# Kernel optimization log

Measured on AMD Instinct MI355X. Metric: run time of the kernel, lower is better.

Reference implementation:

```python
import jax, jax.numpy as jnp
import numpy as np

N_NODES = 1_000_000
N_EDGES = 16_000_000
ALPHA = 0.85
MAX_ITER = 100
TOL = 1e-6


def setup_inputs() -> dict:
    key = jax.random.key(0)
    k1, k2 = jax.random.split(key)
    x = jax.random.normal(k1, (N_NODES,), dtype=jnp.float32)
    edge_index = jax.random.randint(k2, (2, N_EDGES), 0, N_NODES, dtype=jnp.int64)
    return {"x": x, "edge_index": edge_index}


def reference(x, edge_index):
    N = x.shape[0]
    rows = edge_index[0]  # destination (row index of sparse M)
    cols = edge_index[1]  # source (column index; out-degree normalization)

    # values of M*alpha: alpha / out_degree(col), gathered per edge
    deg = jax.ops.segment_sum(jnp.ones_like(cols, dtype=jnp.float32), cols,
                              num_segments=N)  # torch.bincount(columns)
    vals = ALPHA / deg[cols]  # [E]; div-by-zero -> inf, matching torch

    inv_n = jnp.float32(1.0) / N
    teleport = (1.0 - ALPHA) * inv_n
    v0 = jnp.full((N,), inv_n, dtype=jnp.float32)
    thresh = jnp.float32(N) * TOL

    def step(carry, _):
        v, done = carry
        # SpMV: out[row] += vals * v[col]
        new_v = jax.ops.segment_sum(vals * v[cols], rows, num_segments=N) + teleport
        err = jnp.abs(new_v - v).sum()
        v_next = jnp.where(done, v, new_v)
        done_next = done | (err < thresh)
        return (v_next, done_next), None

    (v, _), _ = jax.lax.scan(step, (v0, jnp.array(False)), None, length=MAX_ITER)
    return v
```

## Files before the change

kernel.cpp:

```cpp
#include <hip/hip_runtime.h>
#include <hip/hip_cooperative_groups.h>

namespace cg = cooperative_groups;


static constexpr int   NN       = 1000000;
static constexpr int   NE       = 16000000;
static constexpr float ALPHA    = 0.85f;
static constexpr int   MAX_ITER = 100;
static constexpr float THRESH   = 1.0f;
static constexpr float INV_N    = 1.0f / 1000000.0f;
static constexpr float TELEPORT = 0.15f * (1.0f / 1000000.0f);
static constexpr float SCALE    = 8796093022208.0f;
static constexpr float INVSCALE = 1.0f / 8796093022208.0f;

static constexpr int T     = 256;
static constexpr int T5    = 512;
static constexpr int NCH   = 2048;
static constexpr int BSH   = 14;
static constexpr int BKN   = 16384;
static constexpr int NBK   = 64;
static constexpr int NBKU  = 62;
static constexpr int NSUBB = 496;
static constexpr int NSLC  = 489;
static constexpr int NK4A  = 124;

static constexpr size_t OFF_WCG  = 0;
static constexpr size_t OFF_WR8  = 64002048;
static constexpr size_t OFF_PACC = 80002560;
static constexpr size_t OFF_CNTR = 112508416;
static constexpr size_t OFF_CNTC = 113032704;
static constexpr size_t OFF_CTRL = 113556992;
static constexpr size_t OFF_RDEG = 113561088;
static constexpr size_t OFF_W    = 117561088;
static constexpr size_t NEED     = 121561120;

typedef int      vi4 __attribute__((ext_vector_type(4)));
typedef unsigned vu4 __attribute__((ext_vector_type(4)));

template<typename TT>
__device__ __forceinline__ TT ntload(const TT* p) { return __builtin_nontemporal_load(p); }

struct P {
    unsigned* wcg; unsigned char* wr8; unsigned short* colp;
    int* pacc; unsigned* cntR; unsigned* cntC;
    float* rdeg; float* w;
    unsigned* totR; unsigned* totC; unsigned* baseR; unsigned* baseC;
    unsigned* flags; int* ovf; float* errF;
};
__device__ __forceinline__ P mk(char* ws) {
    P p;
    p.wcg  = (unsigned*)(ws + OFF_WCG);
    p.wr8  = (unsigned char*)(ws + OFF_WR8);
    p.colp = (unsigned short*)(ws + OFF_PACC);
    p.pacc = (int*)(ws + OFF_PACC);
    p.cntR = (unsigned*)(ws + OFF_CNTR);
    p.cntC = (unsigned*)(ws + OFF_CNTC);
    unsigned* ctrl = (unsigned*)(ws + OFF_CTRL);
    p.rdeg = (float*)(ws + OFF_RDEG);
    p.w    = (float*)(ws + OFF_W);
    p.totR = ctrl; p.totC = ctrl + 64; p.baseR = ctrl + 128; p.baseC = ctrl + 200;
    p.flags = ctrl + 280; p.ovf = (int*)(ctrl + 281); p.errF = (float*)(ctrl + 288);
    return p;
}

__device__ void atomic_fallback(cg::grid_group& grid, int is64,
                                const int* e32, const long long* e64,
                                int* ai, int* deg, float* rdeg,
                                float* vA, float* vB, float* w,
                                float* err, float* out,
                                int tid, int stride, int th)
{
    for (int i = tid; i < NN; i += stride) { ai[i] = 0; deg[i] = 0; vA[i] = INV_N; }
    grid.sync();
    if (is64) { const long long* cols = e64 + NE;
        for (int e = tid; e < NE; e += stride) atomicAdd(&deg[(int)cols[e]], 1); }
    else      { const int* cols = e32 + NE;
        for (int e = tid; e < NE; e += stride) atomicAdd(&deg[cols[e]], 1); }
    grid.sync();
    for (int i = tid; i < NN; i += stride) rdeg[i] = ALPHA / (float)deg[i];
    grid.sync();
    float* v = vA; float* nv = vB;
    for (int iter = 0; iter < MAX_ITER; ++iter) {
        for (int i = tid; i < NN; i += stride) { w[i] = v[i] * rdeg[i]; ai[i] = 0; }
        grid.sync();
        if (is64) { const long long* rows = e64; const long long* cols = e64 + NE;
            for (int e = tid; e < NE; e += stride)
                atomicAdd(&ai[(int)rows[e]], __float2int_rn(w[(int)cols[e]] * SCALE)); }
        else { const int* rows = e32; const int* cols = e32 + NE;
            for (int e = tid; e < NE; e += stride)
                atomicAdd(&ai[rows[e]], __float2int_rn(w[cols[e]] * SCALE)); }
        grid.sync();
        float pe = 0.0f;
        for (int i = tid; i < NN; i += stride) {
            float x = TELEPORT + (float)ai[i] * INVSCALE;
            pe += fabsf(x - v[i]); nv[i] = x;
        }
        #pragma unroll
        for (int off = 32; off > 0; off >>= 1) pe += __shfl_down(pe, off, 64);
        if ((th & 63) == 0) unsafeAtomicAdd(&err[iter], pe);
        grid.sync();
        float e = ((volatile float*)err)[iter];
        float* t = v; v = nv; nv = t;
        if (e < THRESH) break;
    }
    for (int i = tid; i < NN; i += stride) out[i] = v[i];
}

__global__ __launch_bounds__(256) void k0_init(const int* __restrict__ e32, char* ws)
{
    P p = mk(ws);
    __shared__ int snz;
    const int th = threadIdx.x;
    if (th == 0) snz = 0;
    __syncthreads();
    if (e32[2 * th + 1] != 0) atomicOr(&snz, 1);
    __syncthreads();
    if (th == 0) { p.flags[0] = (snz == 0) ? 1u : 0u; *p.ovf = 0; p.w[NN] = 0.0f; }
    if (th < MAX_ITER) p.errF[th] = 0.0f;
}

__global__ __launch_bounds__(256, 8) void k1_hist(const int* __restrict__ e32, char* ws)
{
    P p = mk(ws);
    if (p.flags[0]) return;
    __shared__ int h[128];
    const int th = threadIdx.x, blk = blockIdx.x;
    const int e0 = (int)(((long long)NE * blk) >> 11);
    const int e1 = (int)(((long long)NE * (blk + 1)) >> 11);
    if (th < 128) h[th] = 0;
    __syncthreads();
    const vi4* R4 = (const vi4*)e32;
    const vi4* C4 = (const vi4*)(e32 + NE);
    const int qe = (e1 + 3) >> 2;
    for (int q = (e0 >> 2) + th; q < qe; q += T) {
        vi4 R = R4[q], C = C4[q];
        int rr[4] = {R.x, R.y, R.z, R.w}, cc[4] = {C.x, C.y, C.z, C.w};
        #pragma unroll
        for (int j = 0; j < 4; ++j) {
            int e = 4 * q + j;
            if (e >= e0 && e < e1) {
                atomicAdd(&h[rr[j] >> BSH], 1);
                atomicAdd(&h[64 + (cc[j] >> BSH)], 1);
            }
        }
    }
    __syncthreads();
    if (th < 64) {
        p.cntR[(size_t)th * NCH + blk] = (unsigned)h[th];
        p.cntC[(size_t)th * NCH + blk] = (unsigned)h[64 + th];
    }
}

__global__ __launch_bounds__(256, 4) void k2_scan(char* ws)
{
    P p = mk(ws);
    if (p.flags[0]) return;
    __shared__ int S[256];
    const int th = threadIdx.x, blk = blockIdx.x;
    const int side = blk >> 6, b = blk & 63;
    unsigned* cnt = (side ? p.cntC : p.cntR) + (size_t)b * NCH;
    unsigned v[8]; unsigned s = 0;
    #pragma unroll
    for (int i = 0; i < 8; ++i) { v[i] = cnt[8 * th + i]; s += v[i]; }
    S[th] = (int)s; __syncthreads();
    for (int off = 1; off < 256; off <<= 1) {
        int x = (th >= off) ? S[th - off] : 0;
        __syncthreads(); S[th] += x; __syncthreads();
    }
    unsigned run = (unsigned)S[th] - s;
    #pragma unroll
    for (int i = 0; i < 8; ++i) { unsigned t = v[i]; cnt[8 * th + i] = run; run += t; }
    if (th == 255) (side ? p.totC : p.totR)[b] = run;
}

__global__ __launch_bounds__(256) void k2b_bases(char* ws)
{
    P p = mk(ws);
    if (p.flags[0]) return;
    __shared__ int S[128];
    const int th = threadIdx.x;
    unsigned pt = 0;
    if (th < 128) {
        unsigned t = (th < 64) ? p.totR[th] : p.totC[th - 64];
        pt = (t + 7u) & ~7u;
        S[th] = (int)pt;
    }
    __syncthreads();
    for (int off = 1; off < 64; off <<= 1) {
        int x = (th < 128 && (th & 63) >= off) ? S[th - off] : 0;
        __syncthreads(); if (th < 128) S[th] += x; __syncthreads();
    }
    if (th < 64) {
        p.baseR[th] = (unsigned)S[th] - pt;
        if (th == 63) p.baseR[64] = (unsigned)S[63];
    } else if (th < 128) {
        p.baseC[th - 64] = (unsigned)S[th] - pt;
        if (th == 127) p.baseC[64] = (unsigned)S[127];
    }
    __syncthreads();
    if (th < 64) {
        unsigned tot = p.totC[th], bs = p.baseC[th], pp = (tot + 7u) & ~7u;
        for (unsigned i = tot; i < pp; ++i) p.colp[bs + i] = 0;
    }
}

__global__ __launch_bounds__(256, 2) void k3ab_scat(const int* __restrict__ e32, char* ws)
{
    P p = mk(ws);
    if (p.flags[0]) return;
    __shared__ int SH3[14720];
    unsigned short* pcL  = (unsigned short*)SH3;
    int*            wcL  = SH3 + 4096;
    unsigned char*  wr8L = (unsigned char*)(SH3 + 12288);
    int* cFill = SH3 + 14336; int* cFlsh = SH3 + 14400; int* cWpos = SH3 + 14464;
    int* rFill = SH3 + 14528; int* rFlsh = SH3 + 14592; int* rWpos = SH3 + 14656;
    const int th = threadIdx.x, blk = blockIdx.x;
    if (blk < 64 && th == 0) {
        unsigned tot = p.totR[blk], bs = p.baseR[blk], pt = (tot + 7u) & ~7u;
        for (unsigned i = tot; i < pt; ++i) { p.wcg[bs + i] = (unsigned)NN; p.wr8[bs + i] = 0; }
    }
    if (th < 64) {
        cFill[th] = 0; cFlsh[th] = 0;
        cWpos[th] = (int)(p.baseC[th] + p.cntC[(size_t)th * NCH + blk]);
        rFill[th] = 0; rFlsh[th] = 0;
        rWpos[th] = (int)(p.baseR[th] + p.cntR[(size_t)th * NCH + blk]);
    }
    __syncthreads();
    const int e0 = (int)(((long long)NE * blk) >> 11);
    const int e1 = (int)(((long long)NE * (blk + 1)) >> 11);
    const vi4* R4 = (const vi4*)e32;
    const vi4* C4 = (const vi4*)(e32 + NE);
    const int qs = e0 >> 2, qe = (e1 + 3) >> 2;
    vi4 Rcur = {0,0,0,0}, Ccur = {0,0,0,0};
    if (qs + th < qe) { Rcur = R4[qs + th]; Ccur = C4[qs + th]; }
    for (int qb = qs; qb < qe; qb += T) {
        vi4 Rnext = {0,0,0,0}, Cnext = {0,0,0,0};
        { int qn = qb + T + th; if (qn < qe) { Rnext = R4[qn]; Cnext = C4[qn]; } }
        const int q = qb + th;
        if (q < qe) {
            int rr[4] = {Rcur.x, Rcur.y, Rcur.z, Rcur.w};
            int cc[4] = {Ccur.x, Ccur.y, Ccur.z, Ccur.w};
            #pragma unroll
            for (int j = 0; j < 4; ++j) {
                int e = 4 * q + j;
                if (e >= e0 && e < e1) {
                    int cb = cc[j] >> BSH;
                    int ci = atomicAdd(&cFill[cb], 1);
                    pcL[cb * 128 + (ci & 127)] = (unsigned short)(cc[j] & (BKN - 1));
                    int rb = rr[j] >> BSH;
                    int ri = atomicAdd(&rFill[rb], 1);
                    int sl = ri & 127;
                    int rl14 = rr[j] & (BKN - 1);
                    wcL[rb * 128 + sl]  = (cc[j] & 0xFFFFF) | ((rl14 & 0xFFF) << 20);
                    wr8L[rb * 128 + sl] = (unsigned char)(rl14 >> 12);
                }
            }
        }
        __syncthreads();
        const int wv = th >> 6, lane = th & 63;
        for (int k = 0; k < 16; ++k) {
            const int b = wv * 16 + k;
            int ff = cFill[b], fl = cFlsh[b], wp = cWpos[b];
            if (ff - fl > 128) *p.ovf = 1;
            while (ff - fl >= 64) {
                p.colp[wp + lane] = pcL[b * 128 + ((fl + lane) & 127)];
                fl += 64; wp += 64;
            }
            if (lane == 0) { cFlsh[b] = fl; cWpos[b] = wp; }
            ff = rFill[b]; fl = rFlsh[b]; wp = rWpos[b];
            if (ff - fl > 128) *p.ovf = 1;
            while (ff - fl >= 64) {
                p.wcg[wp + lane] = (unsigned)wcL[b * 128 + ((fl + lane) & 127)];
                p.wr8[wp + lane] = wr8L[b * 128 + ((fl + lane) & 127)];
                fl += 64; wp += 64;
            }
            if (lane == 0) { rFlsh[b] = fl; rWpos[b] = wp; }
        }
        __syncthreads();
        Rcur = Rnext; Ccur = Cnext;
    }
    {
        const int wv = th >> 6, lane = th & 63;
        for (int k = 0; k < 16; ++k) {
            const int b = wv * 16 + k;
            int ff = cFill[b], fl = cFlsh[b], wp = cWpos[b];
            while (ff > fl) {
                int n = min(64, ff - fl);
                if (lane < n) p.colp[wp + lane] = pcL[b * 128 + ((fl + lane) & 127)];
                fl += n; wp += n;
            }
            ff = rFill[b]; fl = rFlsh[b]; wp = rWpos[b];
            while (ff > fl) {
                int n = min(64, ff - fl);
                if (lane < n) {
                    p.wcg[wp + lane] = (unsigned)wcL[b * 128 + ((fl + lane) & 127)];
                    p.wr8[wp + lane] = wr8L[b * 128 + ((fl + lane) & 127)];
                }
                fl += n; wp += n;
            }
        }
    }
}

__global__ __launch_bounds__(256, 2) void k4a_deg(char* ws, float* __restrict__ outp)
{
    P p = mk(ws);
    if (p.flags[0] || *p.ovf) return;
    __shared__ int SH[16384];
    const int th = threadIdx.x, blk = blockIdx.x;
    const int b = blk >> 1, sub = blk & 1;
    for (int j = th; j < 16384; j += T) SH[j] = 0;
    __syncthreads();
    const unsigned bs = p.baseC[b], tot = p.totC[b], pt = (tot + 7u) & ~7u;
    const unsigned nq = pt >> 3;
    const unsigned qlo = (nq * (unsigned)sub) >> 1;
    const unsigned qhi = (nq * (unsigned)(sub + 1)) >> 1;
    const vu4* p8 = (const vu4*)p.colp + (bs >> 3);
    for (unsigned q = qlo + th; q < qhi; q += T) {
        vu4 x = ntload(p8 + q);
        atomicAdd(&SH[x.x & 0xFFFFu], 1); atomicAdd(&SH[x.x >> 16], 1);
        atomicAdd(&SH[x.y & 0xFFFFu], 1); atomicAdd(&SH[x.y >> 16], 1);
        atomicAdd(&SH[x.z & 0xFFFFu], 1); atomicAdd(&SH[x.z >> 16], 1);
        atomicAdd(&SH[x.w & 0xFFFFu], 1); atomicAdd(&SH[x.w >> 16], 1);
    }
    __syncthreads();
    unsigned* hp = (unsigned*)((unsigned short*)outp + (size_t)blk * 16384);
    for (int j = th; j < 8192; j += T)
        __builtin_nontemporal_store(
            (unsigned)((SH[2*j] & 0xFFFF) | (SH[2*j+1] << 16)), hp + j);
}

__global__ __launch_bounds__(256, 8) void k4b_merge(char* ws, const float* __restrict__ outp)
{
    P p = mk(ws);
    if (p.flags[0] || *p.ovf) return;
    const int th = threadIdx.x, blk = blockIdx.x;
    const int b = blk >> 3, off = (blk & 7) * 2048;
    const int padC = (int)(((p.totC[b] + 7u) & ~7u) - p.totC[b]);
    const unsigned* h0 = (const unsigned*)((const unsigned short*)outp
                         + (size_t)(2*b) * 16384 + off);
    const unsigned* h1 = (const unsigned*)((const unsigned short*)outp
                         + (size_t)(2*b+1) * 16384 + off);
    for (int g = th; g < 512; g += T) {
        int node = b * BKN + off + 4 * g;
        if (node < NN) {
            unsigned a0 = ntload(h0 + 2*g), a1 = ntload(h0 + 2*g + 1);
            unsigned b0 = ntload(h1 + 2*g), b1 = ntload(h1 + 2*g + 1);
            int d0 = (int)((a0 & 0xFFFFu) + (b0 & 0xFFFFu));
            int d1 = (int)((a0 >> 16) + (b0 >> 16));
            int d2 = (int)((a1 & 0xFFFFu) + (b1 & 0xFFFFu));
            int d3 = (int)((a1 >> 16) + (b1 >> 16));
            if (off == 0 && g == 0) d0 -= padC;
            float r0 = ALPHA / (float)d0;
            float r1 = ALPHA / (float)d1;
            float r2 = ALPHA / (float)d2;
            float r3 = ALPHA / (float)d3;
            float4 rr = {r0, r1, r2, r3};
            *(float4*)&p.rdeg[node] = rr;
            float4 ww = {INV_N * r0, INV_N * r1, INV_N * r2, INV_N * r3};
            *(float4*)&p.w[node] = ww;
        }
    }
}

#define GATH8(G, I, CA, CB, H)                                              \
    G##0 = w[(unsigned)CA.x & 0xFFFFFu];                                    \
    G##1 = w[(unsigned)CA.y & 0xFFFFFu];                                    \
    G##2 = w[(unsigned)CA.z & 0xFFFFFu];                                    \
    G##3 = w[(unsigned)CA.w & 0xFFFFFu];                                    \
    G##4 = w[(unsigned)CB.x & 0xFFFFFu];                                    \
    G##5 = w[(unsigned)CB.y & 0xFFFFFu];                                    \
    G##6 = w[(unsigned)CB.z & 0xFFFFFu];                                    \
    G##7 = w[(unsigned)CB.w & 0xFFFFFu];                                    \
    I##0 = ((unsigned)CA.x >> 20) | ((unsigned)( (H)        & 3ull) << 12); \
    I##1 = ((unsigned)CA.y >> 20) | ((unsigned)(((H) >> 8)  & 3ull) << 12); \
    I##2 = ((unsigned)CA.z >> 20) | ((unsigned)(((H) >> 16) & 3ull) << 12); \
    I##3 = ((unsigned)CA.w >> 20) | ((unsigned)(((H) >> 24) & 3ull) << 12); \
    I##4 = ((unsigned)CB.x >> 20) | ((unsigned)(((H) >> 32) & 3ull) << 12); \
    I##5 = ((unsigned)CB.y >> 20) | ((unsigned)(((H) >> 40) & 3ull) << 12); \
    I##6 = ((unsigned)CB.z >> 20) | ((unsigned)(((H) >> 48) & 3ull) << 12); \
    I##7 = ((unsigned)CB.w >> 20) | ((unsigned)(((H) >> 56) & 3ull) << 12);

#define ATOM8(I, G)                                                         \
    atomicAdd(&SH[I##0], __float2int_rn(G##0 * SCALE));                     \
    atomicAdd(&SH[I##1], __float2int_rn(G##1 * SCALE));                     \
    atomicAdd(&SH[I##2], __float2int_rn(G##2 * SCALE));                     \
    atomicAdd(&SH[I##3], __float2int_rn(G##3 * SCALE));                     \
    atomicAdd(&SH[I##4], __float2int_rn(G##4 * SCALE));                     \
    atomicAdd(&SH[I##5], __float2int_rn(G##5 * SCALE));                     \
    atomicAdd(&SH[I##6], __float2int_rn(G##6 * SCALE));                     \
    atomicAdd(&SH[I##7], __float2int_rn(G##7 * SCALE));

template<int TT>
__device__ __forceinline__ void scatter_phase(const P& p, int* SH, int th, int blk)
{
    const int b = blk >> 3, sub = blk & 7;
    for (int j = th; j < 16384; j += TT) SH[j] = 0;
    __syncthreads();
    const unsigned bs = p.baseR[b], tot = p.totR[b], pt = (tot + 7u) & ~7u;
    const unsigned nq = pt >> 3;
    const unsigned qlo = (nq * (unsigned)sub) >> 3;
    const unsigned qhi = (nq * (unsigned)(sub + 1)) >> 3;
    const vi4* __restrict__ c8 = (const vi4*)p.wcg + (bs >> 2);
    const unsigned long long* __restrict__ h8 =
        (const unsigned long long*)(p.wr8 + bs);
    const float* __restrict__ w = p.w;

    unsigned q = qlo + th;
    vi4 caA = {0,0,0,0}, cbA = {0,0,0,0}, caB = {0,0,0,0}, cbB = {0,0,0,0};
    unsigned long long hA = 0, hB = 0;
    float gA0=0,gA1=0,gA2=0,gA3=0,gA4=0,gA5=0,gA6=0,gA7=0;
    float gB0=0,gB1=0,gB2=0,gB3=0,gB4=0,gB5=0,gB6=0,gB7=0;
    unsigned iA0=0,iA1=0,iA2=0,iA3=0,iA4=0,iA5=0,iA6=0,iA7=0;
    unsigned iB0=0,iB1=0,iB2=0,iB3=0,iB4=0,iB5=0,iB6=0,iB7=0;
    if (q < qhi)      { caA = ntload(c8+2*q);      cbA = ntload(c8+2*q+1);      hA = ntload(h8+q); }
    if (q + TT < qhi) { caB = ntload(c8+2*(q+TT)); cbB = ntload(c8+2*(q+TT)+1); hB = ntload(h8+q+TT); }
    if (q < qhi)      { GATH8(gA, iA, caA, cbA, hA) }
    while (q < qhi) {
        if (q + TT < qhi)   { GATH8(gB, iB, caB, cbB, hB) }
        if (q + 2*TT < qhi) { caA = ntload(c8+2*(q+2*TT)); cbA = ntload(c8+2*(q+2*TT)+1); hA = ntload(h8+q+2*TT); }
        ATOM8(iA, gA)
        q += TT;
        if (q >= qhi) break;
        if (q + TT < qhi)   { GATH8(gA, iA, caA, cbA, hA) }
        if (q + 2*TT < qhi) { caB = ntload(c8+2*(q+2*TT)); cbB = ntload(c8+2*(q+2*TT)+1); hB = ntload(h8+q+2*TT); }
        ATOM8(iB, gB)
        q += TT;
    }
    __syncthreads();
    vi4* pa = (vi4*)(p.pacc + (size_t)blk * 16384);
    const vi4* s4 = (const vi4*)SH;
    for (int j = th; j < 4096; j += TT)
        __builtin_nontemporal_store(s4[j], pa + j);
}

__device__ __forceinline__ void merge_phase(const P& p, float* out, int iter,
                                            int th, int blk, float* sred)
{
    float pe = 0.0f;
    const int b = blk >> 3, off = (blk & 7) * 2048;
    for (int g = th; g < 512; g += T) {
        int node = b * BKN + off + 4 * g;
        if (node < NN) {
            vi4 acc = {0, 0, 0, 0};
            #pragma unroll
            for (int qq = 0; qq < 8; ++qq) {
                const vi4* pp = (const vi4*)(p.pacc + (size_t)(b*8+qq)*16384 + off);
                vi4 x = ntload(pp + g);
                acc.x += x.x; acc.y += x.y; acc.z += x.z; acc.w += x.w;
            }
            float x0 = TELEPORT + (float)acc.x * INVSCALE;
            float x1 = TELEPORT + (float)acc.y * INVSCALE;
            float x2 = TELEPORT + (float)acc.z * INVSCALE;
            float x3 = TELEPORT + (float)acc.w * INVSCALE;
            float4 prev;
            if (iter == 0) prev = make_float4(INV_N, INV_N, INV_N, INV_N);
            else           prev = *(const float4*)&out[node];
            pe += fabsf(x0 - prev.x) + fabsf(x1 - prev.y)
                + fabsf(x2 - prev.z) + fabsf(x3 - prev.w);
            float4 nv = {x0, x1, x2, x3};
            *(float4*)&out[node] = nv;
            float4 rd = *(const float4*)&p.rdeg[node];
            float4 nw = {x0*rd.x, x1*rd.y, x2*rd.z, x3*rd.w};
            *(float4*)&p.w[node] = nw;
        }
    }
    #pragma unroll
    for (int o2 = 32; o2 > 0; o2 >>= 1) pe += __shfl_down(pe, o2, 64);
    if ((th & 63) == 0) sred[th >> 6] = pe;
    __syncthreads();
    if (th == 0)
        unsafeAtomicAdd(&p.errF[iter], sred[0] + sred[1] + sred[2] + sred[3]);
}

__global__ __launch_bounds__(512, 2) void k5a_scatter(char* __restrict__ ws)
{
    P p = mk(ws);
    if (p.flags[0] || *p.ovf) return;
    __shared__ int SH[16384];
    scatter_phase<T5>(p, SH, threadIdx.x, blockIdx.x);
}

__global__ __launch_bounds__(256, 4) void k5b_merge(char* __restrict__ ws,
                                                    float* __restrict__ out)
{
    P p = mk(ws);
    if (p.flags[0] || *p.ovf) return;
    __shared__ float sred[4];
    merge_phase(p, out, 0, threadIdx.x, blockIdx.x, sred);
}

__global__ __launch_bounds__(256, 2)
void k5c_iter(const int* __restrict__ e32, const long long* __restrict__ e64,
              char* __restrict__ ws, float* __restrict__ out)
{
    cg::grid_group grid = cg::this_grid();
    P p = mk(ws);
    const int th = threadIdx.x, blk = blockIdx.x;
    const int tid = blk * T + th;
    const int stride = gridDim.x * T;
    __shared__ int SH[16384];
    __shared__ float sred[4];

    if (p.flags[0] || *p.ovf) {
        atomic_fallback(grid, (int)p.flags[0], e32, e64,
                        (int*)ws, (int*)(ws + (size_t)4*1024*1024), p.rdeg,
                        (float*)(ws + (size_t)8*1024*1024),
                        (float*)(ws + (size_t)12*1024*1024),
                        (float*)(ws + (size_t)16*1024*1024),
                        p.errF, out, tid, stride, th);
        return;
    }

    for (int iter = 1; iter < MAX_ITER; ++iter) {
        const float e = ((volatile float*)p.errF)[iter - 1];
        if (e < THRESH) break;
        if (blk < NSUBB) scatter_phase<T>(p, SH, th, blk);
        grid.sync();
        if (blk < NSLC) merge_phase(p, out, iter, th, blk, sred);
        grid.sync();
    }
}

__global__ __launch_bounds__(256, 4)
void pagerank_atomic(const int* __restrict__ e32, const long long* __restrict__ e64,
                     int* __restrict__ ai, int* __restrict__ deg,
                     float* __restrict__ rdeg, float* __restrict__ vA,
                     float* __restrict__ vB, float* __restrict__ w,
                     float* __restrict__ err, int* __restrict__ flags,
                     float* __restrict__ out)
{
    cg::grid_group grid = cg::this_grid();
    const int tid = blockIdx.x * blockDim.x + threadIdx.x;
    const int stride = gridDim.x * blockDim.x;
    if (tid < MAX_ITER) err[tid] = 0.0f;
    if (tid == 0) {
        int nz = 0;
        for (int k = 1; k < 512; k += 2) nz |= e32[k];
        flags[0] = (nz == 0) ? 1 : 0;
    }
    grid.sync();
    atomic_fallback(grid, flags[0], e32, e64, ai, deg, rdeg, vA, vB, w, err, out,
                    tid, stride, threadIdx.x);
}

extern "C" void kernel_launch(void* const* d_in, const int* in_sizes, int n_in,
                              void* d_out, int out_size, void* d_ws, size_t ws_size,
                              hipStream_t stream)
{
    (void)n_in; (void)out_size; (void)in_sizes;
    const int*       e32 = (const int*)d_in[1];
    const long long* e64 = (const long long*)d_in[1];
    float* out = (float*)d_out;
    char*  ws  = (char*)d_ws;

    int occ = 0;
    hipOccupancyMaxActiveBlocksPerMultiprocessor(&occ, (const void*)k5c_iter, T, 0);

    if (ws_size >= NEED && occ >= 2) {
        k0_init<<<1,    T, 0, stream>>>(e32, ws);
        k1_hist<<<NCH,  T, 0, stream>>>(e32, ws);
        k2_scan<<<128,  T, 0, stream>>>(ws);
        k2b_bases<<<1,  T, 0, stream>>>(ws);
        k3ab_scat<<<NCH, T, 0, stream>>>(e32, ws);
        k4a_deg<<<NK4A, T, 0, stream>>>(ws, out);
        k4b_merge<<<NSLC, T, 0, stream>>>(ws, out);
        k5a_scatter<<<NSUBB, T5, 0, stream>>>(ws);
        k5b_merge<<<NSLC, T, 0, stream>>>(ws, out);
        void* args[] = { (void*)&e32, (void*)&e64, (void*)&ws, (void*)&out };
        hipLaunchCooperativeKernel((const void*)k5c_iter,
                                   dim3(512), dim3(T), args, 0, stream);
        return;
    }

    const size_t MB = 1024 * 1024;
    int*   ai    = (int*)(ws);
    int*   deg   = (int*)(ws + 4 * MB);
    float* rdeg  = (float*)(ws + 8 * MB);
    float* vA    = (float*)(ws + 12 * MB);
    float* vB    = (float*)(ws + 16 * MB);
    float* w     = (float*)(ws + 20 * MB);
    float* err   = (float*)(ws + 24 * MB);
    int*   flg   = (int*)(ws + 24 * MB + 4096);
    int occ2 = 0;
    hipOccupancyMaxActiveBlocksPerMultiprocessor(&occ2, (const void*)pagerank_atomic, 256, 0);
    if (occ2 < 1) occ2 = 1;
    int grid = occ2 * 256; if (grid > 2048) grid = 2048;
    void* args[] = { (void*)&e32, (void*)&e64, (void*)&ai, (void*)&deg, (void*)&rdeg,
                     (void*)&vA, (void*)&vB, (void*)&w, (void*)&err, (void*)&flg,
                     (void*)&out };
    hipLaunchCooperativeKernel((const void*)pagerank_atomic,
                               dim3(grid), dim3(256), args, 0, stream);
}
```

Measured before the change: 545.3 us.

## Replace histogram-scan bucketing with atomic per-bucket cursors into fixed-capacity slots

Removes the histogram, scan and base-computation kernels. The scatter kernel now claims output positions through global atomic cursors per bucket, writing into fixed-capacity slots, and a small pad kernel finalizes the totals. The degree kernel is split across four sub-blocks per bucket and writes its partial histograms to a dedicated workspace region instead of the output buffer. Edge loads use nontemporal hints. The cost is extra atomics, nondeterministic edge order within a bucket, a larger workspace, and an overflow flag that falls back if a bucket exceeds its capacity.

Result: slower. 684.2 us (+25.5%).

```diff
diff --git a/kernel.cpp b/kernel.cpp
--- a/kernel.cpp
+++ b/kernel.cpp
@@ -14,26 +14,25 @@
 static constexpr float SCALE    = 8796093022208.0f;
 static constexpr float INVSCALE = 1.0f / 8796093022208.0f;
 
-static constexpr int T     = 256;
-static constexpr int T5    = 512;
-static constexpr int NCH   = 2048;
-static constexpr int BSH   = 14;
-static constexpr int BKN   = 16384;
-static constexpr int NBK   = 64;
-static constexpr int NBKU  = 62;
-static constexpr int NSUBB = 496;
-static constexpr int NSLC  = 489;
-static constexpr int NK4A  = 124;
+static constexpr int      T     = 256;
+static constexpr int      T5    = 512;
+static constexpr int      NCH   = 2048;
+static constexpr int      BSH   = 14;
+static constexpr int      BKN   = 16384;
+static constexpr int      NBKU  = 62;
+static constexpr int      NSUBB = 496;
+static constexpr int      NSLC  = 489;
+static constexpr int      NK4A  = 248;
+static constexpr unsigned CAP   = 268288;
 
 static constexpr size_t OFF_WCG  = 0;
-static constexpr size_t OFF_WR8  = 64002048;
-static constexpr size_t OFF_PACC = 80002560;
-static constexpr size_t OFF_CNTR = 112508416;
-static constexpr size_t OFF_CNTC = 113032704;
-static constexpr size_t OFF_CTRL = 113556992;
-static constexpr size_t OFF_RDEG = 113561088;
-static constexpr size_t OFF_W    = 117561088;
-static constexpr size_t NEED     = 121561120;
+static constexpr size_t OFF_WR8  = 66535424;
+static constexpr size_t OFF_PACC = 83169280;
+static constexpr size_t OFF_HP   = 116436992;
+static constexpr size_t OFF_CTRL = 124563456;
+static constexpr size_t OFF_RDEG = 124579840;
+static constexpr size_t OFF_W    = 128579840;
+static constexpr size_t NEED     = 132579872;
 
 typedef int      vi4 __attribute__((ext_vector_type(4)));
 typedef unsigned vu4 __attribute__((ext_vector_type(4)));
@@ -43,9 +42,9 @@
 
 struct P {
     unsigned* wcg; unsigned char* wr8; unsigned short* colp;
-    int* pacc; unsigned* cntR; unsigned* cntC;
+    int* pacc; unsigned short* hp;
     float* rdeg; float* w;
-    unsigned* totR; unsigned* totC; unsigned* baseR; unsigned* baseC;
+    unsigned* totR; unsigned* totC; unsigned* curR; unsigned* curC;
     unsigned* flags; int* ovf; float* errF;
 };
 __device__ __forceinline__ P mk(char* ws) {
@@ -54,13 +53,14 @@
     p.wr8  = (unsigned char*)(ws + OFF_WR8);
     p.colp = (unsigned short*)(ws + OFF_PACC);
     p.pacc = (int*)(ws + OFF_PACC);
-    p.cntR = (unsigned*)(ws + OFF_CNTR);
-    p.cntC = (unsigned*)(ws + OFF_CNTC);
+    p.hp   = (unsigned short*)(ws + OFF_HP);
     unsigned* ctrl = (unsigned*)(ws + OFF_CTRL);
     p.rdeg = (float*)(ws + OFF_RDEG);
     p.w    = (float*)(ws + OFF_W);
-    p.totR = ctrl; p.totC = ctrl + 64; p.baseR = ctrl + 128; p.baseC = ctrl + 200;
+    p.totR = ctrl; p.totC = ctrl + 64;
     p.flags = ctrl + 280; p.ovf = (int*)(ctrl + 281); p.errF = (float*)(ctrl + 288);
+    p.curR = ctrl + 1024;
+    p.curC = ctrl + 2048;
     return p;
 }
 
@@ -116,116 +116,23 @@
     __syncthreads();
     if (e32[2 * th + 1] != 0) atomicOr(&snz, 1);
     __syncthreads();
+    if (th < NBKU) { p.curR[th * 16] = 0; p.curC[th * 16] = 0; }
     if (th == 0) { p.flags[0] = (snz == 0) ? 1u : 0u; *p.ovf = 0; p.w[NN] = 0.0f; }
     if (th < MAX_ITER) p.errF[th] = 0.0f;
 }
 
-__global__ __launch_bounds__(256, 8) void k1_hist(const int* __restrict__ e32, char* ws)
+__global__ __launch_bounds__(256, 2) void k3ab_scat(const int* __restrict__ e32, char* ws)
 {
     P p = mk(ws);
     if (p.flags[0]) return;
-    __shared__ int h[128];
-    const int th = threadIdx.x, blk = blockIdx.x;
-    const int e0 = (int)(((long long)NE * blk) >> 11);
-    const int e1 = (int)(((long long)NE * (blk + 1)) >> 11);
-    if (th < 128) h[th] = 0;
-    __syncthreads();
-    const vi4* R4 = (const vi4*)e32;
-    const vi4* C4 = (const vi4*)(e32 + NE);
-    const int qe = (e1 + 3) >> 2;
-    for (int q = (e0 >> 2) + th; q < qe; q += T) {
-        vi4 R = R4[q], C = C4[q];
-        int rr[4] = {R.x, R.y, R.z, R.w}, cc[4] = {C.x, C.y, C.z, C.w};
-        #pragma unroll
-        for (int j = 0; j < 4; ++j) {
-            int e = 4 * q + j;
-            if (e >= e0 && e < e1) {
-                atomicAdd(&h[rr[j] >> BSH], 1);
-                atomicAdd(&h[64 + (cc[j] >> BSH)], 1);
-            }
-        }
-    }
-    __syncthreads();
-    if (th < 64) {
-        p.cntR[(size_t)th * NCH + blk] = (unsigned)h[th];
-        p.cntC[(size_t)th * NCH + blk] = (unsigned)h[64 + th];
-    }
-}
-
-__global__ __launch_bounds__(256, 4) void k2_scan(char* ws)
-{
-    P p = mk(ws);
-    if (p.flags[0]) return;
-    __shared__ int S[256];
-    const int th = threadIdx.x, blk = blockIdx.x;
-    const int side = blk >> 6, b = blk & 63;
-    unsigned* cnt = (side ? p.cntC : p.cntR) + (size_t)b * NCH;
-    unsigned v[8]; unsigned s = 0;
-    #pragma unroll
-    for (int i = 0; i < 8; ++i) { v[i] = cnt[8 * th + i]; s += v[i]; }
-    S[th] = (int)s; __syncthreads();
-    for (int off = 1; off < 256; off <<= 1) {
-        int x = (th >= off) ? S[th - off] : 0;
-        __syncthreads(); S[th] += x; __syncthreads();
-    }
-    unsigned run = (unsigned)S[th] - s;
-    #pragma unroll
-    for (int i = 0; i < 8; ++i) { unsigned t = v[i]; cnt[8 * th + i] = run; run += t; }
-    if (th == 255) (side ? p.totC : p.totR)[b] = run;
-}
-
-__global__ __launch_bounds__(256) void k2b_bases(char* ws)
-{
-    P p = mk(ws);
-    if (p.flags[0]) return;
-    __shared__ int S[128];
-    const int th = threadIdx.x;
-    unsigned pt = 0;
-    if (th < 128) {
-        unsigned t = (th < 64) ? p.totR[th] : p.totC[th - 64];
-        pt = (t + 7u) & ~7u;
-        S[th] = (int)pt;
-    }
-    __syncthreads();
-    for (int off = 1; off < 64; off <<= 1) {
-        int x = (th < 128 && (th & 63) >= off) ? S[th - off] : 0;
-        __syncthreads(); if (th < 128) S[th] += x; __syncthreads();
-    }
-    if (th < 64) {
-        p.baseR[th] = (unsigned)S[th] - pt;
-        if (th == 63) p.baseR[64] = (unsigned)S[63];
-    } else if (th < 128) {
-        p.baseC[th - 64] = (unsigned)S[th] - pt;
-        if (th == 127) p.baseC[64] = (unsigned)S[127];
-    }
-    __syncthreads();
-    if (th < 64) {
-        unsigned tot = p.totC[th], bs = p.baseC[th], pp = (tot + 7u) & ~7u;
-        for (unsigned i = tot; i < pp; ++i) p.colp[bs + i] = 0;
-    }
-}
-
-__global__ __launch_bounds__(256, 2) void k3ab_scat(const int* __restrict__ e32, char* ws)
-{
-    P p = mk(ws);
-    if (p.flags[0]) return;
-    __shared__ int SH3[14720];
+    __shared__ int SH3[14592];
     unsigned short* pcL  = (unsigned short*)SH3;
     int*            wcL  = SH3 + 4096;
     unsigned char*  wr8L = (unsigned char*)(SH3 + 12288);
-    int* cFill = SH3 + 14336; int* cFlsh = SH3 + 14400; int* cWpos = SH3 + 14464;
-    int* rFill = SH3 + 14528; int* rFlsh = SH3 + 14592; int* rWpos = SH3 + 14656;
+    int* cFill = SH3 + 14336; int* cFlsh = SH3 + 14400;
+    int* rFill = SH3 + 14464; int* rFlsh = SH3 + 14528;
     const int th = threadIdx.x, blk = blockIdx.x;
-    if (blk < 64 && th == 0) {
-        unsigned tot = p.totR[blk], bs = p.baseR[blk], pt = (tot + 7u) & ~7u;
-        for (unsigned i = tot; i < pt; ++i) { p.wcg[bs + i] = (unsigned)NN; p.wr8[bs + i] = 0; }
-    }
-    if (th < 64) {
-        cFill[th] = 0; cFlsh[th] = 0;
-        cWpos[th] = (int)(p.baseC[th] + p.cntC[(size_t)th * NCH + blk]);
-        rFill[th] = 0; rFlsh[th] = 0;
-        rWpos[th] = (int)(p.baseR[th] + p.cntR[(size_t)th * NCH + blk]);
-    }
+    if (th < 64) { cFill[th] = 0; cFlsh[th] = 0; rFill[th] = 0; rFlsh[th] = 0; }
     __syncthreads();
     const int e0 = (int)(((long long)NE * blk) >> 11);
     const int e1 = (int)(((long long)NE * (blk + 1)) >> 11);
@@ -233,10 +140,10 @@
     const vi4* C4 = (const vi4*)(e32 + NE);
     const int qs = e0 >> 2, qe = (e1 + 3) >> 2;
     vi4 Rcur = {0,0,0,0}, Ccur = {0,0,0,0};
-    if (qs + th < qe) { Rcur = R4[qs + th]; Ccur = C4[qs + th]; }
+    if (qs + th < qe) { Rcur = ntload(R4 + qs + th); Ccur = ntload(C4 + qs + th); }
     for (int qb = qs; qb < qe; qb += T) {
         vi4 Rnext = {0,0,0,0}, Cnext = {0,0,0,0};
-        { int qn = qb + T + th; if (qn < qe) { Rnext = R4[qn]; Cnext = C4[qn]; } }
+        { int qn = qb + T + th; if (qn < qe) { Rnext = ntload(R4 + qn); Cnext = ntload(C4 + qn); } }
         const int q = qb + th;
         if (q < qe) {
             int rr[4] = {Rcur.x, Rcur.y, Rcur.z, Rcur.w};
@@ -261,21 +168,31 @@
         const int wv = th >> 6, lane = th & 63;
         for (int k = 0; k < 16; ++k) {
             const int b = wv * 16 + k;
-            int ff = cFill[b], fl = cFlsh[b], wp = cWpos[b];
+            int ff = cFill[b], fl = cFlsh[b];
             if (ff - fl > 128) *p.ovf = 1;
             while (ff - fl >= 64) {
-                p.colp[wp + lane] = pcL[b * 128 + ((fl + lane) & 127)];
-                fl += 64; wp += 64;
-            }
-            if (lane == 0) { cFlsh[b] = fl; cWpos[b] = wp; }
-            ff = rFill[b]; fl = rFlsh[b]; wp = rWpos[b];
+                unsigned wp = 0;
+                if (lane == 0) wp = atomicAdd(&p.curC[b * 16], 64u);
+                wp = (unsigned)__shfl((int)wp, 0);
+                if (wp + 64u <= CAP)
+                    p.colp[(size_t)b * CAP + wp + lane] = pcL[b * 128 + ((fl + lane) & 127)];
+                else if (lane == 0) *p.ovf = 1;
+                fl += 64;
+            }
+            if (lane == 0) cFlsh[b] = fl;
+            ff = rFill[b]; fl = rFlsh[b];
             if (ff - fl > 128) *p.ovf = 1;
             while (ff - fl >= 64) {
-                p.wcg[wp + lane] = (unsigned)wcL[b * 128 + ((fl + lane) & 127)];
-                p.wr8[wp + lane] = wr8L[b * 128 + ((fl + lane) & 127)];
-                fl += 64; wp += 64;
-            }
-            if (lane == 0) { rFlsh[b] = fl; rWpos[b] = wp; }
+                unsigned wp = 0;
+                if (lane == 0) wp = atomicAdd(&p.curR[b * 16], 64u);
+                wp = (unsigned)__shfl((int)wp, 0);
+                if (wp + 64u <= CAP) {
+                    p.wcg[(size_t)b * CAP + wp + lane] = (unsigned)wcL[b * 128 + ((fl + lane) & 127)];
+                    p.wr8[(size_t)b * CAP + wp + lane] = wr8L[b * 128 + ((fl + lane) & 127)];
+                } else if (lane == 0) *p.ovf = 1;
+                fl += 64;
+            }
+            if (lane == 0) rFlsh[b] = fl;
         }
         __syncthreads();
         Rcur = Rnext; Ccur = Cnext;
@@ -284,38 +201,70 @@
         const int wv = th >> 6, lane = th & 63;
         for (int k = 0; k < 16; ++k) {
             const int b = wv * 16 + k;
-            int ff = cFill[b], fl = cFlsh[b], wp = cWpos[b];
+            int ff = cFill[b], fl = cFlsh[b];
             while (ff > fl) {
                 int n = min(64, ff - fl);
-                if (lane < n) p.colp[wp + lane] = pcL[b * 128 + ((fl + lane) & 127)];
-                fl += n; wp += n;
-            }
-            ff = rFill[b]; fl = rFlsh[b]; wp = rWpos[b];
+                unsigned wp = 0;
+                if (lane == 0) wp = atomicAdd(&p.curC[b * 16], (unsigned)n);
+                wp = (unsigned)__shfl((int)wp, 0);
+                if (wp + (unsigned)n <= CAP) {
+                    if (lane < n)
+                        p.colp[(size_t)b * CAP + wp + lane] = pcL[b * 128 + ((fl + lane) & 127)];
+                } else if (lane == 0) *p.ovf = 1;
+                fl += n;
+            }
+            ff = rFill[b]; fl = rFlsh[b];
             while (ff > fl) {
                 int n = min(64, ff - fl);
-                if (lane < n) {
-                    p.wcg[wp + lane] = (unsigned)wcL[b * 128 + ((fl + lane) & 127)];
-                    p.wr8[wp + lane] = wr8L[b * 128 + ((fl + lane) & 127)];
-                }
-                fl += n; wp += n;
-            }
-        }
-    }
-}
-
-__global__ __launch_bounds__(256, 2) void k4a_deg(char* ws, float* __restrict__ outp)
+                unsigned wp = 0;
+                if (lane == 0) wp = atomicAdd(&p.curR[b * 16], (unsigned)n);
+                wp = (unsigned)__shfl((int)wp, 0);
+                if (wp + (unsigned)n <= CAP) {
+                    if (lane < n) {
+                        p.wcg[(size_t)b * CAP + wp + lane] = (unsigned)wcL[b * 128 + ((fl + lane) & 127)];
+                        p.wr8[(size_t)b * CAP + wp + lane] = wr8L[b * 128 + ((fl + lane) & 127)];
+                    }
+                } else if (lane == 0) *p.ovf = 1;
+                fl += n;
+            }
+        }
+    }
+}
+
+__global__ __launch_bounds__(128) void k3p_pad(char* ws)
+{
+    P p = mk(ws);
+    if (p.flags[0]) return;
+    const int th = threadIdx.x;
+    if (th < NBKU) {
+        unsigned tot = p.curC[th * 16], pt = (tot + 7u) & ~7u;
+        if (pt > CAP) *p.ovf = 1;
+        else for (unsigned i = tot; i < pt; ++i) p.colp[(size_t)th * CAP + i] = 0;
+        p.totC[th] = tot;
+        tot = p.curR[th * 16]; pt = (tot + 7u) & ~7u;
+        if (pt > CAP) *p.ovf = 1;
+        else for (unsigned i = tot; i < pt; ++i) {
+            p.wcg[(size_t)th * CAP + i] = (unsigned)NN;
+            p.wr8[(size_t)th * CAP + i] = 0;
+        }
+        p.totR[th] = tot;
+    }
+}
+
+__global__ __launch_bounds__(256, 2) void k4a_deg(char* ws)
 {
     P p = mk(ws);
     if (p.flags[0] || *p.ovf) return;
     __shared__ int SH[16384];
     const int th = threadIdx.x, blk = blockIdx.x;
-    const int b = blk >> 1, sub = blk & 1;
+    const int b = blk >> 2, sub = blk & 3;
     for (int j = th; j < 16384; j += T) SH[j] = 0;
     __syncthreads();
-    const unsigned bs = p.baseC[b], tot = p.totC[b], pt = (tot + 7u) & ~7u;
+    const unsigned bs = (unsigned)b * CAP;
+    const unsigned tot = p.totC[b], pt = (tot + 7u) & ~7u;
     const unsigned nq = pt >> 3;
-    const unsigned qlo = (nq * (unsigned)sub) >> 1;
-    const unsigned qhi = (nq * (unsigned)(sub + 1)) >> 1;
+    const unsigned qlo = (nq * (unsigned)sub) >> 2;
+    const unsigned qhi = (nq * (unsigned)(sub + 1)) >> 2;
     const vu4* p8 = (const vu4*)p.colp + (bs >> 3);
     for (unsigned q = qlo + th; q < qhi; q += T) {
         vu4 x = ntload(p8 + q);
@@ -325,32 +274,30 @@
         atomicAdd(&SH[x.w & 0xFFFFu], 1); atomicAdd(&SH[x.w >> 16], 1);
     }
     __syncthreads();
-    unsigned* hp = (unsigned*)((unsigned short*)outp + (size_t)blk * 16384);
+    unsigned* hp = (unsigned*)(p.hp + (size_t)blk * 16384);
     for (int j = th; j < 8192; j += T)
         __builtin_nontemporal_store(
             (unsigned)((SH[2*j] & 0xFFFF) | (SH[2*j+1] << 16)), hp + j);
 }
 
-__global__ __launch_bounds__(256, 8) void k4b_merge(char* ws, const float* __restrict__ outp)
+__global__ __launch_bounds__(256, 8) void k4b_merge(char* ws)
 {
     P p = mk(ws);
     if (p.flags[0] || *p.ovf) return;
     const int th = threadIdx.x, blk = blockIdx.x;
     const int b = blk >> 3, off = (blk & 7) * 2048;
     const int padC = (int)(((p.totC[b] + 7u) & ~7u) - p.totC[b]);
-    const unsigned* h0 = (const unsigned*)((const unsigned short*)outp
-                         + (size_t)(2*b) * 16384 + off);
-    const unsigned* h1 = (const unsigned*)((const unsigned short*)outp
-                         + (size_t)(2*b+1) * 16384 + off);
     for (int g = th; g < 512; g += T) {
         int node = b * BKN + off + 4 * g;
         if (node < NN) {
-            unsigned a0 = ntload(h0 + 2*g), a1 = ntload(h0 + 2*g + 1);
-            unsigned b0 = ntload(h1 + 2*g), b1 = ntload(h1 + 2*g + 1);
-            int d0 = (int)((a0 & 0xFFFFu) + (b0 & 0xFFFFu));
-            int d1 = (int)((a0 >> 16) + (b0 >> 16));
-            int d2 = (int)((a1 & 0xFFFFu) + (b1 & 0xFFFFu));
-            int d3 = (int)((a1 >> 16) + (b1 >> 16));
+            int d0 = 0, d1 = 0, d2 = 0, d3 = 0;
+            #pragma unroll
+            for (int qq = 0; qq < 4; ++qq) {
+                const unsigned* h = (const unsigned*)(p.hp + (size_t)(4*b+qq) * 16384 + off);
+                unsigned a0 = ntload(h + 2*g), a1 = ntload(h + 2*g + 1);
+                d0 += (int)(a0 & 0xFFFFu); d1 += (int)(a0 >> 16);
+                d2 += (int)(a1 & 0xFFFFu); d3 += (int)(a1 >> 16);
+            }
             if (off == 0 && g == 0) d0 -= padC;
             float r0 = ALPHA / (float)d0;
             float r1 = ALPHA / (float)d1;
@@ -398,7 +345,8 @@
     const int b = blk >> 3, sub = blk & 7;
     for (int j = th; j < 16384; j += TT) SH[j] = 0;
     __syncthreads();
-    const unsigned bs = p.baseR[b], tot = p.totR[b], pt = (tot + 7u) & ~7u;
+    const unsigned bs = (unsigned)b * CAP;
+    const unsigned tot = p.totR[b], pt = (tot + 7u) & ~7u;
     const unsigned nq = pt >> 3;
     const unsigned qlo = (nq * (unsigned)sub) >> 3;
     const unsigned qhi = (nq * (unsigned)(sub + 1)) >> 3;
@@ -559,13 +507,11 @@
     hipOccupancyMaxActiveBlocksPerMultiprocessor(&occ, (const void*)k5c_iter, T, 0);
 
     if (ws_size >= NEED && occ >= 2) {
-        k0_init<<<1,    T, 0, stream>>>(e32, ws);
-        k1_hist<<<NCH,  T, 0, stream>>>(e32, ws);
-        k2_scan<<<128,  T, 0, stream>>>(ws);
-        k2b_bases<<<1,  T, 0, stream>>>(ws);
+        k0_init<<<1,     T, 0, stream>>>(e32, ws);
         k3ab_scat<<<NCH, T, 0, stream>>>(e32, ws);
-        k4a_deg<<<NK4A, T, 0, stream>>>(ws, out);
-        k4b_merge<<<NSLC, T, 0, stream>>>(ws, out);
+        k3p_pad<<<1,   128, 0, stream>>>(ws);
+        k4a_deg<<<NK4A,  T, 0, stream>>>(ws);
+        k4b_merge<<<NSLC,T, 0, stream>>>(ws);
         k5a_scatter<<<NSUBB, T5, 0, stream>>>(ws);
         k5b_merge<<<NSLC, T, 0, stream>>>(ws, out);
         void* args[] = { (void*)&e32, (void*)&e64, (void*)&ws, (void*)&out };
```
